# Performance work log

Hardware: AMD Instinct MI355X
Metric: run time of the kernel (lower is better)

Reference implementation:

```python
import jax, jax.numpy as jnp
import numpy as np

GCN_DIM, GEO_DIM, HIDDEN_DIM, TOWER_DIM, RECENT_K = 128, 32, 256, 128, 50
NUM_ITEMS, NUM_USERS = 100000, 16384


def _normalize(x, eps=1e-12):
    # torch F.normalize(dim=1): x / max(||x||, eps)
    n = jnp.linalg.norm(x, axis=1, keepdims=True)
    return x / jnp.maximum(n, eps)


def setup_inputs() -> dict:
    key = jax.random.key(0)
    ks = jax.random.split(key, 16)
    s = 0.05  # weight init scale
    return {
        "item_feat": jax.random.normal(ks[0], (NUM_ITEMS, 2), jnp.float32),
        "gcn_item_emb": jax.random.normal(ks[1], (NUM_ITEMS, GCN_DIM), jnp.float32),
        "gcn_user_emb": jax.random.normal(ks[2], (NUM_USERS, GCN_DIM), jnp.float32),
        "user_items": jax.random.randint(ks[3], (NUM_USERS, RECENT_K), 0, NUM_ITEMS, jnp.int32),
        "Wg": s * jax.random.normal(ks[4], (2, GEO_DIM), jnp.float32),
        "bg": jnp.zeros((GEO_DIM,), jnp.float32),
        "Wi1": s * jax.random.normal(ks[5], (GCN_DIM + GEO_DIM, HIDDEN_DIM), jnp.float32),
        "bi1": jnp.zeros((HIDDEN_DIM,), jnp.float32),
        "Wi2": s * jax.random.normal(ks[6], (HIDDEN_DIM, TOWER_DIM), jnp.float32),
        "bi2": jnp.zeros((TOWER_DIM,), jnp.float32),
        "Wq": s * jax.random.normal(ks[7], (GCN_DIM, TOWER_DIM), jnp.float32),
        "bq": jnp.zeros((TOWER_DIM,), jnp.float32),
        "Wk": s * jax.random.normal(ks[8], (TOWER_DIM, TOWER_DIM), jnp.float32),
        "bk": jnp.zeros((TOWER_DIM,), jnp.float32),
        "Wu1": s * jax.random.normal(ks[9], (GCN_DIM + TOWER_DIM, HIDDEN_DIM), jnp.float32),
        "bu1": jnp.zeros((HIDDEN_DIM,), jnp.float32),
        "Wu2": s * jax.random.normal(ks[10], (HIDDEN_DIM, TOWER_DIM), jnp.float32),
        "bu2": jnp.zeros((TOWER_DIM,), jnp.float32),
    }


def reference(item_feat, gcn_item_emb, gcn_user_emb, user_items,
              Wg, bg, Wi1, bi1, Wi2, bi2, Wq, bq, Wk, bk, Wu1, bu1, Wu2, bu2):
    # ---- encode_items ----
    geo = jax.nn.relu(item_feat @ Wg + bg)                       # [I, GEO]
    xi = jnp.concatenate([geo, gcn_item_emb], axis=1)            # [I, GEO+GCN]
    item_emb = _normalize(jax.nn.relu(xi @ Wi1 + bi1) @ Wi2 + bi2)  # [I, T]

    # ---- encode_users (batched ragged attention pooling) ----
    h = item_emb[user_items]                                     # [U, K, T] gather
    q = gcn_user_emb @ Wq + bq                                   # [U, T]
    k = h @ Wk + bk                                              # [U, K, T]
    scores = jnp.einsum('ut,ukt->uk', q, k)                      # [U, K]
    alpha = jax.nn.softmax(scores, axis=1)                       # softmax over history
    rep = jnp.einsum('uk,ukt->ut', alpha, h)                     # [U, T]
    fused = jnp.concatenate([gcn_user_emb, rep], axis=1)         # [U, GCN+T]
    user_emb = _normalize(jax.nn.relu(fused @ Wu1 + bu1) @ Wu2 + bu2)  # [U, T]

    return jnp.concatenate([item_emb, user_emb], axis=0)         # [I+U, T]
```

## Files before the change

kernel.cpp:

```cpp
#include <hip/hip_runtime.h>
#include <hip/hip_bf16.h>
#include <math.h>

#define NITEMS 100000
#define NUSERS 16384
#define GCN 128
#define GEO 32
#define HIDD 256
#define TD 128
#define RK 50

typedef unsigned int uint;
typedef unsigned short ushort;
typedef __bf16 bf16x8 __attribute__((ext_vector_type(8)));
typedef float f32x4 __attribute__((ext_vector_type(4)));

__device__ __forceinline__ ushort bfb(float x) {
  union { __hip_bfloat16 b; ushort u; } t; t.b = __float2bfloat16(x); return t.u;
}
__device__ __forceinline__ uint packbf2(float a, float b) {
  return (uint)bfb(a) | ((uint)bfb(b) << 16);
}
__device__ __forceinline__ float bflo(uint d) { return __uint_as_float(d << 16); }
__device__ __forceinline__ float bfhi(uint d) { return __uint_as_float(d & 0xffff0000u); }

union U4B { uint4 u; bf16x8 b; };
__device__ __forceinline__ bf16x8 ldfrag(const ushort* p) { U4B t; t.u = *(const uint4*)p; return t.b; }
__device__ __forceinline__ bf16x8 pack8(float4 a0, float4 a1) {
  U4B t;
  t.u.x = packbf2(a0.x, a0.y); t.u.y = packbf2(a0.z, a0.w);
  t.u.z = packbf2(a1.x, a1.y); t.u.w = packbf2(a1.z, a1.w);
  return t.b;
}

__global__ __launch_bounds__(256) void prep_all(
    const float* __restrict__ Wi1, const float* __restrict__ Wi2,
    const float* __restrict__ Wu1, const float* __restrict__ Wu2,
    const float* __restrict__ Wq, const float* __restrict__ Wk,
    const float* __restrict__ bq,
    ushort* __restrict__ Wi1P, ushort* __restrict__ Wi2P,
    ushort* __restrict__ Wu1P, ushort* __restrict__ Wu2P,
    float* __restrict__ WqkS, float* __restrict__ bqk)
{
  int id = blockIdx.x * 256 + threadIdx.x;
  if (id < 40960) {
    int k = id >> 8, c = id & 255;
    Wi1P[(k >> 5) * 8192 + c * 32 + (k & 31)] = bfb(Wi1[id]);
  } else if (id < 73728) {
    int i = id - 40960; int k = i >> 7, c = i & 127;
    Wi2P[(k >> 5) * 4096 + c * 32 + (k & 31)] = bfb(Wi2[i]);
  } else if (id < 139264) {
    int i = id - 73728; int k = i >> 8, c = i & 255;
    Wu1P[(k >> 5) * 8192 + c * 32 + (k & 31)] = bfb(Wu1[i]);
  } else if (id < 172032) {
    int i = id - 139264; int k = i >> 7, c = i & 127;
    Wu2P[(k >> 5) * 4096 + c * 32 + (k & 31)] = bfb(Wu2[i]);
  } else if (id < 188416) {
    int i = id - 172032; int g = i >> 7, s = i & 127;
    float acc = 0.f;
    for (int t = 0; t < 128; t += 4) {
      float4 a = *(const float4*)(Wq + g * 128 + t);
      float4 b = *(const float4*)(Wk + s * 128 + t);
      acc += a.x * b.x + a.y * b.y + a.z * b.z + a.w * b.w;
    }
    WqkS[g * 128 + s] = acc;
  } else if (id < 188544) {
    int s = id - 188416;
    float acc = 0.f;
    for (int t = 0; t < 128; t += 4) {
      float4 a = *(const float4*)(bq + t);
      float4 b = *(const float4*)(Wk + s * 128 + t);
      acc += a.x * b.x + a.y * b.y + a.z * b.z + a.w * b.w;
    }
    bqk[s] = acc;
  }
}

template <int ROWS, int K1, bool ITEM>
__global__ __launch_bounds__(256, 4) void mlp_kernel(
    const float* __restrict__ xmain,
    const float* __restrict__ feat,
    const float* __restrict__ Wg, const float* __restrict__ bg,
    const ushort* __restrict__ repB,
    const ushort* __restrict__ W1P, const float* __restrict__ b1,
    const ushort* __restrict__ W2P, const float* __restrict__ b2,
    float* __restrict__ outp, ushort* __restrict__ outb)
{
  constexpr int RF = ROWS / 16;
  constexpr int K1CH = K1 / 32;
  __shared__ __align__(16) ushort s_h[ROWS * 264];
  __shared__ float s_red[ROWS * 4];
  __shared__ float s_inv[ROWS];

  const int tid = threadIdx.x;
  const int wid = tid >> 6, lane = tid & 63, g = lane >> 4, q = lane & 15;
  const int i0 = blockIdx.x * ROWS;

  f32x4 acc[RF][4];
  #pragma unroll
  for (int cf = 0; cf < 4; ++cf) {
    float bv = b1[wid * 64 + cf * 16 + q];
    f32x4 t = {bv, bv, bv, bv};
    #pragma unroll
    for (int rf = 0; rf < RF; ++rf) acc[rf][cf] = t;
  }
  const ushort* bbase1 = W1P + (wid * 64 + q) * 32 + g * 8;

  #pragma unroll
  for (int kb = 0; kb < K1CH; ++kb) {
    bf16x8 af[RF], bfr[4];
    if (ITEM && kb == 0) {
      float4 w0a = *(const float4*)(Wg + g * 8),      w0b = *(const float4*)(Wg + g * 8 + 4);
      float4 w1a = *(const float4*)(Wg + 32 + g * 8), w1b = *(const float4*)(Wg + 32 + g * 8 + 4);
      float4 ba  = *(const float4*)(bg + g * 8),      bb = *(const float4*)(bg + g * 8 + 4);
      #pragma unroll
      for (int rf = 0; rf < RF; ++rf) {
        int row = i0 + q + 16 * rf;
        float2 f = *(const float2*)(feat + 2 * (size_t)row);
        float4 lo, hi;
        lo.x = fmaxf(fmaf(f.x, w0a.x, fmaf(f.y, w1a.x, ba.x)), 0.f);
        lo.y = fmaxf(fmaf(f.x, w0a.y, fmaf(f.y, w1a.y, ba.y)), 0.f);
        lo.z = fmaxf(fmaf(f.x, w0a.z, fmaf(f.y, w1a.z, ba.z)), 0.f);
        lo.w = fmaxf(fmaf(f.x, w0a.w, fmaf(f.y, w1a.w, ba.w)), 0.f);
        hi.x = fmaxf(fmaf(f.x, w0b.x, fmaf(f.y, w1b.x, bb.x)), 0.f);
        hi.y = fmaxf(fmaf(f.x, w0b.y, fmaf(f.y, w1b.y, bb.y)), 0.f);
        hi.z = fmaxf(fmaf(f.x, w0b.z, fmaf(f.y, w1b.z, bb.z)), 0.f);
        hi.w = fmaxf(fmaf(f.x, w0b.w, fmaf(f.y, w1b.w, bb.w)), 0.f);
        af[rf] = pack8(lo, hi);
      }
    } else if (!ITEM && kb >= K1CH - 4) {
      #pragma unroll
      for (int rf = 0; rf < RF; ++rf) {
        U4B t;
        t.u = *(const uint4*)(repB + (size_t)(i0 + q + 16 * rf) * TD + (kb - (K1CH - 4)) * 32 + g * 8);
        af[rf] = t.b;
      }
    } else {
      const int col = (ITEM ? (kb - 1) : kb) * 32 + g * 8;
      #pragma unroll
      for (int rf = 0; rf < RF; ++rf) {
        const float* rp = xmain + (size_t)(i0 + q + 16 * rf) * GCN + col;
        af[rf] = pack8(*(const float4*)rp, *(const float4*)(rp + 4));
      }
    }
    #pragma unroll
    for (int cf = 0; cf < 4; ++cf) bfr[cf] = ldfrag(bbase1 + kb * 8192 + cf * 512);
    #pragma unroll
    for (int rf = 0; rf < RF; ++rf)
      #pragma unroll
      for (int cf = 0; cf < 4; ++cf)
        acc[rf][cf] = __builtin_amdgcn_mfma_f32_16x16x32_bf16(af[rf], bfr[cf], acc[rf][cf], 0, 0, 0);
  }

  #pragma unroll
  for (int rf = 0; rf < RF; ++rf)
    #pragma unroll
    for (int cf = 0; cf < 4; ++cf)
      #pragma unroll
      for (int e = 0; e < 4; ++e)
        s_h[(16 * rf + 4 * g + e) * 264 + wid * 64 + cf * 16 + q] = bfb(fmaxf(acc[rf][cf][e], 0.f));
  __syncthreads();

  f32x4 acc2[RF][2];
  #pragma unroll
  for (int cf = 0; cf < 2; ++cf) {
    float bv = b2[wid * 32 + cf * 16 + q];
    f32x4 t = {bv, bv, bv, bv};
    #pragma unroll
    for (int rf = 0; rf < RF; ++rf) acc2[rf][cf] = t;
  }
  {
    const ushort* bbase2 = W2P + (wid * 32 + q) * 32 + g * 8;
    #pragma unroll
    for (int kb = 0; kb < 8; ++kb) {
      bf16x8 af[RF], bf2[2];
      #pragma unroll
      for (int rf = 0; rf < RF; ++rf) af[rf] = ldfrag(&s_h[(16 * rf + q) * 264 + kb * 32 + g * 8]);
      #pragma unroll
      for (int cf = 0; cf < 2; ++cf) bf2[cf] = ldfrag(bbase2 + kb * 4096 + cf * 512);
      #pragma unroll
      for (int rf = 0; rf < RF; ++rf)
        #pragma unroll
        for (int cf = 0; cf < 2; ++cf)
          acc2[rf][cf] = __builtin_amdgcn_mfma_f32_16x16x32_bf16(af[rf], bf2[cf], acc2[rf][cf], 0, 0, 0);
    }
  }

  #pragma unroll
  for (int rf = 0; rf < RF; ++rf) {
    #pragma unroll
    for (int e = 0; e < 4; ++e) {
      float p = acc2[rf][0][e] * acc2[rf][0][e] + acc2[rf][1][e] * acc2[rf][1][e];
      p += __shfl_xor(p, 1, 16); p += __shfl_xor(p, 2, 16);
      p += __shfl_xor(p, 4, 16); p += __shfl_xor(p, 8, 16);
      if (q == 0) s_red[(16 * rf + 4 * g + e) * 4 + wid] = p;
    }
  }
  __syncthreads();
  if (tid < ROWS) {
    float s = s_red[tid * 4] + s_red[tid * 4 + 1] + s_red[tid * 4 + 2] + s_red[tid * 4 + 3];
    s_inv[tid] = 1.f / fmaxf(sqrtf(s), 1e-12f);
  }
  __syncthreads();

  #pragma unroll
  for (int rf = 0; rf < RF; ++rf) {
    #pragma unroll
    for (int e = 0; e < 4; ++e) {
      int row = 16 * rf + 4 * g + e;
      int grow = i0 + row;
      float sc = s_inv[row];
      #pragma unroll
      for (int cf = 0; cf < 2; ++cf) {
        float v = acc2[rf][cf][e] * sc;
        outp[(size_t)grow * TD + wid * 32 + cf * 16 + q] = v;
        if constexpr (ITEM) outb[(size_t)grow * TD + wid * 32 + cf * 16 + q] = bfb(v);
      }
    }
  }
}

__global__ __launch_bounds__(256) void qt_kernel(
    const float* __restrict__ gcn_user, const float* __restrict__ WqkS,
    const float* __restrict__ bqk, float* __restrict__ qt)
{
  __shared__ float s_gue[16 * 132];
  const int tid = threadIdx.x;
  const int u0 = blockIdx.x * 16;
  #pragma unroll
  for (int r = 0; r < 8; ++r) {
    int lin = r * 256 + tid;
    int u = lin >> 7, c = lin & 127;
    s_gue[u * 132 + c] = gcn_user[(size_t)(u0 + u) * GCN + c];
  }
  __syncthreads();
  const int ul = tid >> 4, tx = tid & 15, c0 = tx * 8;
  float a[8];
  { float4 b4 = *(const float4*)(bqk + c0); float4 b5 = *(const float4*)(bqk + c0 + 4);
    a[0]=b4.x; a[1]=b4.y; a[2]=b4.z; a[3]=b4.w; a[4]=b5.x; a[5]=b5.y; a[6]=b5.z; a[7]=b5.w; }
  for (int g = 0; g < 128; ++g) {
    float x = s_gue[ul * 132 + g];
    float4 w4 = *(const float4*)(WqkS + g * 128 + c0);
    float4 w5 = *(const float4*)(WqkS + g * 128 + c0 + 4);
    a[0] = fmaf(x, w4.x, a[0]); a[1] = fmaf(x, w4.y, a[1]);
    a[2] = fmaf(x, w4.z, a[2]); a[3] = fmaf(x, w4.w, a[3]);
    a[4] = fmaf(x, w5.x, a[4]); a[5] = fmaf(x, w5.y, a[5]);
    a[6] = fmaf(x, w5.z, a[6]); a[7] = fmaf(x, w5.w, a[7]);
  }
  float* op = qt + (size_t)(u0 + ul) * TD + c0;
  *(float4*)op = make_float4(a[0], a[1], a[2], a[3]);
  *(float4*)(op + 4) = make_float4(a[4], a[5], a[6], a[7]);
}

__global__ __launch_bounds__(256) void attn_kernel(
    const int* __restrict__ user_items, const float* __restrict__ qt,
    const ushort* __restrict__ itemB, ushort* __restrict__ repB)
{
  __shared__ int s_idx[4][52];
  const int tid = threadIdx.x;
  const int wid = tid >> 6, lane = tid & 63, g = lane >> 4, q = lane & 15;
  const int u = blockIdx.x * 4 + wid;
  const int c0 = q * 8;

  if (lane < 52) s_idx[wid][lane] = (lane < 50) ? user_items[(size_t)u * RK + lane] : 0;
  float qv[8];
  { float4 a = *(const float4*)(qt + (size_t)u * TD + c0);
    float4 b = *(const float4*)(qt + (size_t)u * TD + c0 + 4);
    qv[0]=a.x; qv[1]=a.y; qv[2]=a.z; qv[3]=a.w; qv[4]=b.x; qv[5]=b.y; qv[6]=b.z; qv[7]=b.w; }

  uint4 h[13]; float sc[13];
  #pragma unroll
  for (int i = 0; i < 13; ++i) {
    int j = 4 * i + g;
    int idx = s_idx[wid][j];
    h[i] = *(const uint4*)(itemB + (size_t)idx * TD + c0);
    float p = bflo(h[i].x) * qv[0] + bfhi(h[i].x) * qv[1]
            + bflo(h[i].y) * qv[2] + bfhi(h[i].y) * qv[3]
            + bflo(h[i].z) * qv[4] + bfhi(h[i].z) * qv[5]
            + bflo(h[i].w) * qv[6] + bfhi(h[i].w) * qv[7];
    p += __shfl_xor(p, 1, 16); p += __shfl_xor(p, 2, 16);
    p += __shfl_xor(p, 4, 16); p += __shfl_xor(p, 8, 16);
    sc[i] = (j < RK) ? p : -3.0e38f;
  }
  float m = sc[0];
  #pragma unroll
  for (int i = 1; i < 13; ++i) m = fmaxf(m, sc[i]);
  m = fmaxf(m, __shfl_xor(m, 16, 64));
  m = fmaxf(m, __shfl_xor(m, 32, 64));
  float ssum = 0.f;
  #pragma unroll
  for (int i = 0; i < 13; ++i) { sc[i] = __expf(sc[i] - m); ssum += sc[i]; }
  ssum += __shfl_xor(ssum, 16, 64);
  ssum += __shfl_xor(ssum, 32, 64);
  const float inv = 1.f / ssum;
  float rep[8] = {0, 0, 0, 0, 0, 0, 0, 0};
  #pragma unroll
  for (int i = 0; i < 13; ++i) {
    float a = sc[i] * inv;
    rep[0] = fmaf(a, bflo(h[i].x), rep[0]); rep[1] = fmaf(a, bfhi(h[i].x), rep[1]);
    rep[2] = fmaf(a, bflo(h[i].y), rep[2]); rep[3] = fmaf(a, bfhi(h[i].y), rep[3]);
    rep[4] = fmaf(a, bflo(h[i].z), rep[4]); rep[5] = fmaf(a, bfhi(h[i].z), rep[5]);
    rep[6] = fmaf(a, bflo(h[i].w), rep[6]); rep[7] = fmaf(a, bfhi(h[i].w), rep[7]);
  }
  #pragma unroll
  for (int c = 0; c < 8; ++c) {
    rep[c] += __shfl_xor(rep[c], 16, 64);
    rep[c] += __shfl_xor(rep[c], 32, 64);
  }
  if (g == 0) {
    uint4 o;
    o.x = packbf2(rep[0], rep[1]); o.y = packbf2(rep[2], rep[3]);
    o.z = packbf2(rep[4], rep[5]); o.w = packbf2(rep[6], rep[7]);
    *(uint4*)(repB + (size_t)u * TD + c0) = o;
  }
}

extern "C" void kernel_launch(void* const* d_in, const int* in_sizes, int n_in,
                              void* d_out, int out_size, void* d_ws, size_t ws_size,
                              hipStream_t stream) {
  const float* item_feat  = (const float*)d_in[0];
  const float* gcn_item   = (const float*)d_in[1];
  const float* gcn_user   = (const float*)d_in[2];
  const int*   user_items = (const int*)  d_in[3];
  const float* Wg  = (const float*)d_in[4];
  const float* bg  = (const float*)d_in[5];
  const float* Wi1 = (const float*)d_in[6];
  const float* bi1 = (const float*)d_in[7];
  const float* Wi2 = (const float*)d_in[8];
  const float* bi2 = (const float*)d_in[9];
  const float* Wq  = (const float*)d_in[10];
  const float* bq  = (const float*)d_in[11];
  const float* Wk  = (const float*)d_in[12];
  const float* Wu1 = (const float*)d_in[14];
  const float* bu1 = (const float*)d_in[15];
  const float* Wu2 = (const float*)d_in[16];
  const float* bu2 = (const float*)d_in[17];
  float* out = (float*)d_out;

  char* ws = (char*)d_ws;
  ushort* Wi1P  = (ushort*)(ws + 0);
  ushort* Wi2P  = (ushort*)(ws + 81920);
  ushort* Wu1P  = (ushort*)(ws + 147456);
  ushort* Wu2P  = (ushort*)(ws + 278528);
  float*  WqkS  = (float*) (ws + 344064);
  float*  bqk   = (float*) (ws + 409600);
  float*  qtb   = (float*) (ws + 410112);
  ushort* itemB = (ushort*)(ws + 8798720);
  ushort* repB  = (ushort*)(ws + 34398720);

  prep_all<<<737, 256, 0, stream>>>(Wi1, Wi2, Wu1, Wu2, Wq, Wk, bq,
                                    Wi1P, Wi2P, Wu1P, Wu2P, WqkS, bqk);
  qt_kernel<<<NUSERS / 16, 256, 0, stream>>>(gcn_user, WqkS, bqk, qtb);
  mlp_kernel<32, 160, true><<<NITEMS / 32, 256, 0, stream>>>(
      gcn_item, item_feat, Wg, bg, nullptr, Wi1P, bi1, Wi2P, bi2, out, itemB);
  attn_kernel<<<NUSERS / 4, 256, 0, stream>>>(user_items, qtb, itemB, repB);
  mlp_kernel<32, 256, false><<<NUSERS / 32, 256, 0, stream>>>(
      gcn_user, nullptr, Wg, bg, repB, Wu1P, bu1, Wu2P, bu2, out + (size_t)NITEMS * TD, nullptr);
}
```

Measured before the change: 151.9 us.

## Make item MLP persistent with register-resident weights and double-buffered input prefetch

The item MLP becomes a persistent kernel with a fixed grid of 512 blocks looping over 32-row tiles. Each block loads its W1/W2 bf16 fragments into registers once and prefetches the next tile's gcn_item rows and features into a double-buffered shared-memory staging area while the current tile computes. The user MLP is split into its own kernel that also keeps W1 fragments in registers, and bf16 packing now uses native casts. The aim is to cut repeated weight loads and hide global load latency, at the cost of more registers and lower occupancy (launch bounds 256,2).

```diff
diff --git a/kernel.cpp b/kernel.cpp
--- a/kernel.cpp
+++ b/kernel.cpp
@@ -9,6 +9,8 @@
 #define HIDD 256
 #define TD 128
 #define RK 50
+#define NT_I (NITEMS / 32)
+#define GRID_I 512
 
 typedef unsigned int uint;
 typedef unsigned short ushort;
@@ -26,11 +28,11 @@
 
 union U4B { uint4 u; bf16x8 b; };
 __device__ __forceinline__ bf16x8 ldfrag(const ushort* p) { U4B t; t.u = *(const uint4*)p; return t.b; }
-__device__ __forceinline__ bf16x8 pack8(float4 a0, float4 a1) {
-  U4B t;
-  t.u.x = packbf2(a0.x, a0.y); t.u.y = packbf2(a0.z, a0.w);
-  t.u.z = packbf2(a1.x, a1.y); t.u.w = packbf2(a1.z, a1.w);
-  return t.b;
+__device__ __forceinline__ bf16x8 pack8c(float4 a0, float4 a1) {
+  bf16x8 r;
+  r[0] = (__bf16)a0.x; r[1] = (__bf16)a0.y; r[2] = (__bf16)a0.z; r[3] = (__bf16)a0.w;
+  r[4] = (__bf16)a1.x; r[5] = (__bf16)a1.y; r[6] = (__bf16)a1.z; r[7] = (__bf16)a1.w;
+  return r;
 }
 
 __global__ __launch_bounds__(256) void prep_all(
@@ -76,84 +78,248 @@
   }
 }
 
-template <int ROWS, int K1, bool ITEM>
-__global__ __launch_bounds__(256, 4) void mlp_kernel(
-    const float* __restrict__ xmain,
-    const float* __restrict__ feat,
+__global__ __launch_bounds__(256, 2) void item_mlp(
+    const float* __restrict__ gcn_item, const float* __restrict__ feat,
     const float* __restrict__ Wg, const float* __restrict__ bg,
-    const ushort* __restrict__ repB,
     const ushort* __restrict__ W1P, const float* __restrict__ b1,
     const ushort* __restrict__ W2P, const float* __restrict__ b2,
     float* __restrict__ outp, ushort* __restrict__ outb)
 {
-  constexpr int RF = ROWS / 16;
-  constexpr int K1CH = K1 / 32;
-  __shared__ __align__(16) ushort s_h[ROWS * 264];
-  __shared__ float s_red[ROWS * 4];
-  __shared__ float s_inv[ROWS];
+  __shared__ __align__(16) float  s_x[2][32 * 132];
+  __shared__ __align__(16) ushort s_h[32 * 264];
+  __shared__ float s_red[32 * 4];
+  __shared__ float s_inv[32];
 
   const int tid = threadIdx.x;
   const int wid = tid >> 6, lane = tid & 63, g = lane >> 4, q = lane & 15;
-  const int i0 = blockIdx.x * ROWS;
-
-  f32x4 acc[RF][4];
+
+  bf16x8 wb1[5][4], wb2[8][2];
+  #pragma unroll
+  for (int kb = 0; kb < 5; ++kb)
+    #pragma unroll
+    for (int cf = 0; cf < 4; ++cf)
+      wb1[kb][cf] = ldfrag(W1P + kb * 8192 + (wid * 64 + cf * 16 + q) * 32 + g * 8);
+  #pragma unroll
+  for (int kb = 0; kb < 8; ++kb)
+    #pragma unroll
+    for (int cf = 0; cf < 2; ++cf)
+      wb2[kb][cf] = ldfrag(W2P + kb * 4096 + (wid * 32 + cf * 16 + q) * 32 + g * 8);
+
+  float bv1[4], bv2[2];
+  #pragma unroll
+  for (int cf = 0; cf < 4; ++cf) bv1[cf] = b1[wid * 64 + cf * 16 + q];
+  #pragma unroll
+  for (int cf = 0; cf < 2; ++cf) bv2[cf] = b2[wid * 32 + cf * 16 + q];
+
+  const float4 w0a = *(const float4*)(Wg + g * 8),      w0b = *(const float4*)(Wg + g * 8 + 4);
+  const float4 w1a = *(const float4*)(Wg + 32 + g * 8), w1b = *(const float4*)(Wg + 32 + g * 8 + 4);
+  const float4 ba  = *(const float4*)(bg + g * 8),      bb = *(const float4*)(bg + g * 8 + 4);
+
+  float4 stg[4];
+  float2 fc0, fc1, fn0, fn1;
+  {
+    const int i0 = blockIdx.x * 32;
+    #pragma unroll
+    for (int i = 0; i < 4; ++i) {
+      int f = i * 256 + tid, row = f >> 5, c4 = (f & 31) * 4;
+      stg[i] = *(const float4*)(gcn_item + (size_t)(i0 + row) * GCN + c4);
+    }
+    fc0 = *(const float2*)(feat + 2 * (size_t)(i0 + q));
+    fc1 = *(const float2*)(feat + 2 * (size_t)(i0 + q + 16));
+    #pragma unroll
+    for (int i = 0; i < 4; ++i) {
+      int f = i * 256 + tid, row = f >> 5, c4 = (f & 31) * 4;
+      *(float4*)(&s_x[0][row * 132 + c4]) = stg[i];
+    }
+  }
+
+  int cur = 0;
+  for (int t = blockIdx.x; t < NT_I; t += GRID_I) {
+    const int tn = t + GRID_I;
+    const bool hn = tn < NT_I;
+    if (hn) {
+      const int i0n = tn * 32;
+      #pragma unroll
+      for (int i = 0; i < 4; ++i) {
+        int f = i * 256 + tid, row = f >> 5, c4 = (f & 31) * 4;
+        stg[i] = *(const float4*)(gcn_item + (size_t)(i0n + row) * GCN + c4);
+      }
+      fn0 = *(const float2*)(feat + 2 * (size_t)(i0n + q));
+      fn1 = *(const float2*)(feat + 2 * (size_t)(i0n + q + 16));
+    }
+    __syncthreads();
+
+    f32x4 acc[2][4];
+    #pragma unroll
+    for (int cf = 0; cf < 4; ++cf) {
+      f32x4 tv = {bv1[cf], bv1[cf], bv1[cf], bv1[cf]};
+      acc[0][cf] = tv; acc[1][cf] = tv;
+    }
+    #pragma unroll
+    for (int kb = 0; kb < 5; ++kb) {
+      bf16x8 af[2];
+      if (kb == 0) {
+        float4 lo, hi;
+        lo.x = fmaxf(fmaf(fc0.x, w0a.x, fmaf(fc0.y, w1a.x, ba.x)), 0.f);
+        lo.y = fmaxf(fmaf(fc0.x, w0a.y, fmaf(fc0.y, w1a.y, ba.y)), 0.f);
+        lo.z = fmaxf(fmaf(fc0.x, w0a.z, fmaf(fc0.y, w1a.z, ba.z)), 0.f);
+        lo.w = fmaxf(fmaf(fc0.x, w0a.w, fmaf(fc0.y, w1a.w, ba.w)), 0.f);
+        hi.x = fmaxf(fmaf(fc0.x, w0b.x, fmaf(fc0.y, w1b.x, bb.x)), 0.f);
+        hi.y = fmaxf(fmaf(fc0.x, w0b.y, fmaf(fc0.y, w1b.y, bb.y)), 0.f);
+        hi.z = fmaxf(fmaf(fc0.x, w0b.z, fmaf(fc0.y, w1b.z, bb.z)), 0.f);
+        hi.w = fmaxf(fmaf(fc0.x, w0b.w, fmaf(fc0.y, w1b.w, bb.w)), 0.f);
+        af[0] = pack8c(lo, hi);
+        lo.x = fmaxf(fmaf(fc1.x, w0a.x, fmaf(fc1.y, w1a.x, ba.x)), 0.f);
+        lo.y = fmaxf(fmaf(fc1.x, w0a.y, fmaf(fc1.y, w1a.y, ba.y)), 0.f);
+        lo.z = fmaxf(fmaf(fc1.x, w0a.z, fmaf(fc1.y, w1a.z, ba.z)), 0.f);
+        lo.w = fmaxf(fmaf(fc1.x, w0a.w, fmaf(fc1.y, w1a.w, ba.w)), 0.f);
+        hi.x = fmaxf(fmaf(fc1.x, w0b.x, fmaf(fc1.y, w1b.x, bb.x)), 0.f);
+        hi.y = fmaxf(fmaf(fc1.x, w0b.y, fmaf(fc1.y, w1b.y, bb.y)), 0.f);
+        hi.z = fmaxf(fmaf(fc1.x, w0b.z, fmaf(fc1.y, w1b.z, bb.z)), 0.f);
+        hi.w = fmaxf(fmaf(fc1.x, w0b.w, fmaf(fc1.y, w1b.w, bb.w)), 0.f);
+        af[1] = pack8c(lo, hi);
+      } else {
+        #pragma unroll
+        for (int rf = 0; rf < 2; ++rf) {
+          const float* rp = &s_x[cur][(q + 16 * rf) * 132 + (kb - 1) * 32 + g * 8];
+          af[rf] = pack8c(*(const float4*)rp, *(const float4*)(rp + 4));
+        }
+      }
+      #pragma unroll
+      for (int rf = 0; rf < 2; ++rf)
+        #pragma unroll
+        for (int cf = 0; cf < 4; ++cf)
+          acc[rf][cf] = __builtin_amdgcn_mfma_f32_16x16x32_bf16(af[rf], wb1[kb][cf], acc[rf][cf], 0, 0, 0);
+    }
+
+    if (hn) {
+      #pragma unroll
+      for (int i = 0; i < 4; ++i) {
+        int f = i * 256 + tid, row = f >> 5, c4 = (f & 31) * 4;
+        *(float4*)(&s_x[cur ^ 1][row * 132 + c4]) = stg[i];
+      }
+    }
+
+    #pragma unroll
+    for (int rf = 0; rf < 2; ++rf)
+      #pragma unroll
+      for (int cf = 0; cf < 4; ++cf)
+        #pragma unroll
+        for (int e = 0; e < 4; ++e)
+          s_h[(16 * rf + 4 * g + e) * 264 + wid * 64 + cf * 16 + q] = bfb(fmaxf(acc[rf][cf][e], 0.f));
+    __syncthreads();
+
+    f32x4 acc2[2][2];
+    #pragma unroll
+    for (int cf = 0; cf < 2; ++cf) {
+      f32x4 tv = {bv2[cf], bv2[cf], bv2[cf], bv2[cf]};
+      acc2[0][cf] = tv; acc2[1][cf] = tv;
+    }
+    #pragma unroll
+    for (int kb = 0; kb < 8; ++kb) {
+      bf16x8 af[2];
+      #pragma unroll
+      for (int rf = 0; rf < 2; ++rf) af[rf] = ldfrag(&s_h[(16 * rf + q) * 264 + kb * 32 + g * 8]);
+      #pragma unroll
+      for (int rf = 0; rf < 2; ++rf)
+        #pragma unroll
+        for (int cf = 0; cf < 2; ++cf)
+          acc2[rf][cf] = __builtin_amdgcn_mfma_f32_16x16x32_bf16(af[rf], wb2[kb][cf], acc2[rf][cf], 0, 0, 0);
+    }
+
+    #pragma unroll
+    for (int rf = 0; rf < 2; ++rf) {
+      #pragma unroll
+      for (int e = 0; e < 4; ++e) {
+        float p = acc2[rf][0][e] * acc2[rf][0][e] + acc2[rf][1][e] * acc2[rf][1][e];
+        p += __shfl_xor(p, 1, 16); p += __shfl_xor(p, 2, 16);
+        p += __shfl_xor(p, 4, 16); p += __shfl_xor(p, 8, 16);
+        if (q == 0) s_red[(16 * rf + 4 * g + e) * 4 + wid] = p;
+      }
+    }
+    __syncthreads();
+    if (tid < 32) {
+      float s = s_red[tid * 4] + s_red[tid * 4 + 1] + s_red[tid * 4 + 2] + s_red[tid * 4 + 3];
+      s_inv[tid] = 1.f / fmaxf(sqrtf(s), 1e-12f);
+    }
+    __syncthreads();
+
+    {
+      const int i0 = t * 32;
+      #pragma unroll
+      for (int rf = 0; rf < 2; ++rf) {
+        #pragma unroll
+        for (int e = 0; e < 4; ++e) {
+          int row = 16 * rf + 4 * g + e;
+          float sc = s_inv[row];
+          #pragma unroll
+          for (int cf = 0; cf < 2; ++cf) {
+            float v = acc2[rf][cf][e] * sc;
+            outp[(size_t)(i0 + row) * TD + wid * 32 + cf * 16 + q] = v;
+            outb[(size_t)(i0 + row) * TD + wid * 32 + cf * 16 + q] = bfb(v);
+          }
+        }
+      }
+    }
+    fc0 = fn0; fc1 = fn1;
+    cur ^= 1;
+  }
+}
+
+__global__ __launch_bounds__(256, 2) void user_mlp(
+    const float* __restrict__ gcn_user, const ushort* __restrict__ repB,
+    const ushort* __restrict__ W1P, const float* __restrict__ b1,
+    const ushort* __restrict__ W2P, const float* __restrict__ b2,
+    float* __restrict__ outp)
+{
+  __shared__ __align__(16) ushort s_h[32 * 264];
+  __shared__ float s_red[32 * 4];
+  __shared__ float s_inv[32];
+
+  const int tid = threadIdx.x;
+  const int wid = tid >> 6, lane = tid & 63, g = lane >> 4, q = lane & 15;
+  const int i0 = blockIdx.x * 32;
+
+  bf16x8 wb1[8][4];
+  #pragma unroll
+  for (int kb = 0; kb < 8; ++kb)
+    #pragma unroll
+    for (int cf = 0; cf < 4; ++cf)
+      wb1[kb][cf] = ldfrag(W1P + kb * 8192 + (wid * 64 + cf * 16 + q) * 32 + g * 8);
+
+  f32x4 acc[2][4];
   #pragma unroll
   for (int cf = 0; cf < 4; ++cf) {
     float bv = b1[wid * 64 + cf * 16 + q];
-    f32x4 t = {bv, bv, bv, bv};
-    #pragma unroll
-    for (int rf = 0; rf < RF; ++rf) acc[rf][cf] = t;
-  }
-  const ushort* bbase1 = W1P + (wid * 64 + q) * 32 + g * 8;
-
-  #pragma unroll
-  for (int kb = 0; kb < K1CH; ++kb) {
-    bf16x8 af[RF], bfr[4];
-    if (ITEM && kb == 0) {
-      float4 w0a = *(const float4*)(Wg + g * 8),      w0b = *(const float4*)(Wg + g * 8 + 4);
-      float4 w1a = *(const float4*)(Wg + 32 + g * 8), w1b = *(const float4*)(Wg + 32 + g * 8 + 4);
-      float4 ba  = *(const float4*)(bg + g * 8),      bb = *(const float4*)(bg + g * 8 + 4);
-      #pragma unroll
-      for (int rf = 0; rf < RF; ++rf) {
-        int row = i0 + q + 16 * rf;
-        float2 f = *(const float2*)(feat + 2 * (size_t)row);
-        float4 lo, hi;
-        lo.x = fmaxf(fmaf(f.x, w0a.x, fmaf(f.y, w1a.x, ba.x)), 0.f);
-        lo.y = fmaxf(fmaf(f.x, w0a.y, fmaf(f.y, w1a.y, ba.y)), 0.f);
-        lo.z = fmaxf(fmaf(f.x, w0a.z, fmaf(f.y, w1a.z, ba.z)), 0.f);
-        lo.w = fmaxf(fmaf(f.x, w0a.w, fmaf(f.y, w1a.w, ba.w)), 0.f);
-        hi.x = fmaxf(fmaf(f.x, w0b.x, fmaf(f.y, w1b.x, bb.x)), 0.f);
-        hi.y = fmaxf(fmaf(f.x, w0b.y, fmaf(f.y, w1b.y, bb.y)), 0.f);
-        hi.z = fmaxf(fmaf(f.x, w0b.z, fmaf(f.y, w1b.z, bb.z)), 0.f);
-        hi.w = fmaxf(fmaf(f.x, w0b.w, fmaf(f.y, w1b.w, bb.w)), 0.f);
-        af[rf] = pack8(lo, hi);
-      }
-    } else if (!ITEM && kb >= K1CH - 4) {
-      #pragma unroll
-      for (int rf = 0; rf < RF; ++rf) {
+    f32x4 tv = {bv, bv, bv, bv};
+    acc[0][cf] = tv; acc[1][cf] = tv;
+  }
+  #pragma unroll
+  for (int kb = 0; kb < 8; ++kb) {
+    bf16x8 af[2];
+    if (kb < 4) {
+      #pragma unroll
+      for (int rf = 0; rf < 2; ++rf) {
+        const float* rp = gcn_user + (size_t)(i0 + q + 16 * rf) * GCN + kb * 32 + g * 8;
+        af[rf] = pack8c(*(const float4*)rp, *(const float4*)(rp + 4));
+      }
+    } else {
+      #pragma unroll
+      for (int rf = 0; rf < 2; ++rf) {
         U4B t;
-        t.u = *(const uint4*)(repB + (size_t)(i0 + q + 16 * rf) * TD + (kb - (K1CH - 4)) * 32 + g * 8);
+        t.u = *(const uint4*)(repB + (size_t)(i0 + q + 16 * rf) * TD + (kb - 4) * 32 + g * 8);
         af[rf] = t.b;
       }
-    } else {
-      const int col = (ITEM ? (kb - 1) : kb) * 32 + g * 8;
-      #pragma unroll
-      for (int rf = 0; rf < RF; ++rf) {
-        const float* rp = xmain + (size_t)(i0 + q + 16 * rf) * GCN + col;
-        af[rf] = pack8(*(const float4*)rp, *(const float4*)(rp + 4));
-      }
-    }
-    #pragma unroll
-    for (int cf = 0; cf < 4; ++cf) bfr[cf] = ldfrag(bbase1 + kb * 8192 + cf * 512);
-    #pragma unroll
-    for (int rf = 0; rf < RF; ++rf)
+    }
+    #pragma unroll
+    for (int rf = 0; rf < 2; ++rf)
       #pragma unroll
       for (int cf = 0; cf < 4; ++cf)
-        acc[rf][cf] = __builtin_amdgcn_mfma_f32_16x16x32_bf16(af[rf], bfr[cf], acc[rf][cf], 0, 0, 0);
-  }
-
-  #pragma unroll
-  for (int rf = 0; rf < RF; ++rf)
+        acc[rf][cf] = __builtin_amdgcn_mfma_f32_16x16x32_bf16(af[rf], wb1[kb][cf], acc[rf][cf], 0, 0, 0);
+  }
+
+  #pragma unroll
+  for (int rf = 0; rf < 2; ++rf)
     #pragma unroll
     for (int cf = 0; cf < 4; ++cf)
       #pragma unroll
@@ -161,25 +327,24 @@
         s_h[(16 * rf + 4 * g + e) * 264 + wid * 64 + cf * 16 + q] = bfb(fmaxf(acc[rf][cf][e], 0.f));
   __syncthreads();
 
-  f32x4 acc2[RF][2];
+  f32x4 acc2[2][2];
   #pragma unroll
   for (int cf = 0; cf < 2; ++cf) {
     float bv = b2[wid * 32 + cf * 16 + q];
-    f32x4 t = {bv, bv, bv, bv};
-    #pragma unroll
-    for (int rf = 0; rf < RF; ++rf) acc2[rf][cf] = t;
+    f32x4 tv = {bv, bv, bv, bv};
+    acc2[0][cf] = tv; acc2[1][cf] = tv;
   }
   {
     const ushort* bbase2 = W2P + (wid * 32 + q) * 32 + g * 8;
     #pragma unroll
     for (int kb = 0; kb < 8; ++kb) {
-      bf16x8 af[RF], bf2[2];
-      #pragma unroll
-      for (int rf = 0; rf < RF; ++rf) af[rf] = ldfrag(&s_h[(16 * rf + q) * 264 + kb * 32 + g * 8]);
+      bf16x8 af[2], bf2[2];
+      #pragma unroll
+      for (int rf = 0; rf < 2; ++rf) af[rf] = ldfrag(&s_h[(16 * rf + q) * 264 + kb * 32 + g * 8]);
       #pragma unroll
       for (int cf = 0; cf < 2; ++cf) bf2[cf] = ldfrag(bbase2 + kb * 4096 + cf * 512);
       #pragma unroll
-      for (int rf = 0; rf < RF; ++rf)
+      for (int rf = 0; rf < 2; ++rf)
         #pragma unroll
         for (int cf = 0; cf < 2; ++cf)
           acc2[rf][cf] = __builtin_amdgcn_mfma_f32_16x16x32_bf16(af[rf], bf2[cf], acc2[rf][cf], 0, 0, 0);
@@ -187,7 +352,7 @@
   }
 
   #pragma unroll
-  for (int rf = 0; rf < RF; ++rf) {
+  for (int rf = 0; rf < 2; ++rf) {
     #pragma unroll
     for (int e = 0; e < 4; ++e) {
       float p = acc2[rf][0][e] * acc2[rf][0][e] + acc2[rf][1][e] * acc2[rf][1][e];
@@ -197,25 +362,20 @@
     }
   }
   __syncthreads();
-  if (tid < ROWS) {
+  if (tid < 32) {
     float s = s_red[tid * 4] + s_red[tid * 4 + 1] + s_red[tid * 4 + 2] + s_red[tid * 4 + 3];
     s_inv[tid] = 1.f / fmaxf(sqrtf(s), 1e-12f);
   }
   __syncthreads();
-
-  #pragma unroll
-  for (int rf = 0; rf < RF; ++rf) {
+  #pragma unroll
+  for (int rf = 0; rf < 2; ++rf) {
     #pragma unroll
     for (int e = 0; e < 4; ++e) {
       int row = 16 * rf + 4 * g + e;
-      int grow = i0 + row;
       float sc = s_inv[row];
       #pragma unroll
-      for (int cf = 0; cf < 2; ++cf) {
-        float v = acc2[rf][cf][e] * sc;
-        outp[(size_t)grow * TD + wid * 32 + cf * 16 + q] = v;
-        if constexpr (ITEM) outb[(size_t)grow * TD + wid * 32 + cf * 16 + q] = bfb(v);
-      }
+      for (int cf = 0; cf < 2; ++cf)
+        outp[(size_t)(i0 + row) * TD + wid * 32 + cf * 16 + q] = acc2[rf][cf][e] * sc;
     }
   }
 }
@@ -351,9 +511,9 @@
   prep_all<<<737, 256, 0, stream>>>(Wi1, Wi2, Wu1, Wu2, Wq, Wk, bq,
                                     Wi1P, Wi2P, Wu1P, Wu2P, WqkS, bqk);
   qt_kernel<<<NUSERS / 16, 256, 0, stream>>>(gcn_user, WqkS, bqk, qtb);
-  mlp_kernel<32, 160, true><<<NITEMS / 32, 256, 0, stream>>>(
-      gcn_item, item_feat, Wg, bg, nullptr, Wi1P, bi1, Wi2P, bi2, out, itemB);
+  item_mlp<<<GRID_I, 256, 0, stream>>>(
+      gcn_item, item_feat, Wg, bg, Wi1P, bi1, Wi2P, bi2, out, itemB);
   attn_kernel<<<NUSERS / 4, 256, 0, stream>>>(user_items, qtb, itemB, repB);
-  mlp_kernel<32, 256, false><<<NUSERS / 32, 256, 0, stream>>>(
-      gcn_user, nullptr, Wg, bg, repB, Wu1P, bu1, Wu2P, bu2, out + (size_t)NITEMS * TD, nullptr);
-}
+  user_mlp<<<NUSERS / 32, 256, 0, stream>>>(
+      gcn_user, repB, Wu1P, bu1, Wu2P, bu2, out + (size_t)NITEMS * TD);
+}
```

After: 173.2 us. 1.14x slower.
